# Optimization experiments

Measured on AMD Instinct MI355X. Metric: run time of the kernel, lower is better.

The kernel has to match this reference:

```python
import jax, jax.numpy as jnp
import numpy as np

N_ATOMS = 512
BATCH = 32


def _get_segments(n):
    # shifted pairs (k, k+1), all combinations of 2 rows, drop pairs where end1 == start2
    pairs = np.stack([np.arange(n - 1), np.arange(1, n)], axis=1)  # (n-1, 2)
    i, j = np.triu_indices(n - 1, k=1)
    seg = np.concatenate([pairs[i], pairs[j]], axis=1)  # (M, 4)
    seg = seg[seg[:, 1] != seg[:, 2]]
    return seg.astype(np.int32)  # (129795, 4) for n=512


def setup_inputs() -> dict:
    key = jax.random.key(0)
    x = jax.random.normal(key, (BATCH, N_ATOMS, 3), dtype=jnp.float32) * 5.0
    segments = jnp.asarray(_get_segments(N_ATOMS))
    return {"x": x, "segments": segments}


def _nnorm(v):
    return v / jnp.linalg.norm(v, axis=-1, keepdims=True)


def reference(x, segments):
    n = N_ATOMS
    x = x.reshape(-1, n, 3)
    B = x.shape[0]
    smat = x[:, segments]                       # (B, S, 4, 3) gather
    S = smat.shape[1]
    # displacements between the two segment endpoints pairs: d_{ab} = p_{2+b} - p_a
    disp = _nnorm((-smat[:, :, :2, None, :] + smat[:, :, None, 2:, :]).reshape(B, S, 4, 3))
    crosses = _nnorm(jnp.cross(disp[:, :, [0, 1, 3, 2]], disp[:, :, [1, 3, 2, 0]]))
    omega = jnp.arcsin(
        jnp.clip(jnp.sum(crosses * crosses[:, :, [1, 2, 3, 0]], axis=-1), -1.0, 1.0)
    ).sum(axis=2)                               # (B, S)
    signs = jnp.sign(
        jnp.sum(
            jnp.cross(_nnorm(smat[:, :, 3] - smat[:, :, 2]), _nnorm(smat[:, :, 1] - smat[:, :, 0]))
            * disp[:, :, 0],
            axis=-1,
        )
    )
    wr = (omega * signs) / (2.0 * jnp.pi)       # (B, S)
    # scatter into adjacency matrix (sequential sets: second overrides first, like torch)
    adj = jnp.zeros((B, n, n), dtype=x.dtype)
    adj = adj.at[:, segments[:, 0], segments[:, 2]].set(wr)
    adj = adj.at[:, segments[:, 1], segments[:, 3]].set(wr)
    return adj + jnp.swapaxes(adj, 1, 2)
```

## Files before the change

### kernel.cpp

```cpp
#include <hip/hip_runtime.h>
#include <math.h>

#define N 512
#define TILE 32
#define TSTRIDE 34
#define INV2PI 0.15915494309189535f

__device__ __forceinline__ float2 pset(float a, float b) { return make_float2(a, b); }
__device__ __forceinline__ float2 psplat(float a) { return make_float2(a, a); }
__device__ __forceinline__ float2 p_sub(float2 a, float2 b) { return make_float2(a.x - b.x, a.y - b.y); }
__device__ __forceinline__ float2 p_mul(float2 a, float2 b) { return make_float2(a.x * b.x, a.y * b.y); }
__device__ __forceinline__ float2 p_fma(float2 a, float2 b, float2 c) {
    return make_float2(fmaf(a.x, b.x, c.x), fmaf(a.y, b.y, c.y));
}
__device__ __forceinline__ float2 p_fmsub(float2 a, float2 b, float2 c, float2 d) {
    return make_float2(fmaf(a.x, b.x, -(c.x * d.x)), fmaf(a.y, b.y, -(c.y * d.y)));
}
__device__ __forceinline__ float2 p_rsq(float2 a) {
    return make_float2(__builtin_amdgcn_rsqf(a.x), __builtin_amdgcn_rsqf(a.y));
}

struct F3P { float2 x, y, z; };

__device__ __forceinline__ F3P pp_sub(F3P a, F3P b) {
    return {p_sub(a.x, b.x), p_sub(a.y, b.y), p_sub(a.z, b.z)};
}
__device__ __forceinline__ F3P pp_cross(F3P a, F3P b) {
    F3P c;
    c.x = p_fmsub(a.y, b.z, a.z, b.y);
    c.y = p_fmsub(a.z, b.x, a.x, b.z);
    c.z = p_fmsub(a.x, b.y, a.y, b.x);
    return c;
}
__device__ __forceinline__ float2 pp_dot(F3P a, F3P b) {
    return p_fma(a.x, b.x, p_fma(a.y, b.y, p_mul(a.z, b.z)));
}

__device__ __forceinline__ float2 p_asin_clamped(float2 t) {
    float2 ax = make_float2(fminf(fabsf(t.x), 1.f), fminf(fabsf(t.y), 1.f));
    float2 p = p_fma(ax, psplat(-0.0187293f), psplat(0.0742610f));
    p = p_fma(ax, p, psplat(-0.2121144f));
    p = p_fma(ax, p, psplat(1.5707288f));
    float sx = __builtin_amdgcn_sqrtf(1.0f - ax.x);
    float sy = __builtin_amdgcn_sqrtf(1.0f - ax.y);
    float rx = fmaf(-sx, p.x, 1.5707963267948966f);
    float ry = fmaf(-sy, p.y, 1.5707963267948966f);
    return make_float2(copysignf(rx, t.x), copysignf(ry, t.y));
}

__device__ __forceinline__ float2 wr_core2(F3P p0, F3P p1, F3P p2, F3P p3) {
    F3P u = pp_sub(p1, p0);
    F3P v = pp_sub(p3, p2);
    F3P d0 = pp_sub(p2, p0);

    F3P c0 = pp_cross(d0, v);
    F3P c3 = pp_cross(d0, u);
    F3P w  = pp_cross(u, v);
    F3P c1 = {p_sub(w.x, c3.x), p_sub(w.y, c3.y), p_sub(w.z, c3.z)};
    F3P c2 = {p_sub(w.x, c0.x), p_sub(w.y, c0.y), p_sub(w.z, c0.z)};

    float2 svn = pp_dot(w, d0);

    float2 q0 = pp_dot(c0, c0);
    float2 q1 = pp_dot(c1, c1);
    float2 q2 = pp_dot(c2, c2);
    float2 q3 = pp_dot(c3, c3);

    float2 t01 = p_mul(pp_dot(c0, c1), p_rsq(p_mul(q0, q1)));
    float2 t12 = p_mul(pp_dot(c1, c2), p_rsq(p_mul(q1, q2)));
    float2 t23 = p_mul(pp_dot(c2, c3), p_rsq(p_mul(q2, q3)));
    float2 t30 = p_mul(pp_dot(c3, c0), p_rsq(p_mul(q3, q0)));

    float2 a01 = p_asin_clamped(t01), a12 = p_asin_clamped(t12);
    float2 a23 = p_asin_clamped(t23), a30 = p_asin_clamped(t30);
    float2 omega = make_float2(a01.x + a12.x + a23.x + a30.x,
                               a01.y + a12.y + a23.y + a30.y);

    float ox = __int_as_float(__float_as_int(omega.x) ^
                              (__float_as_int(svn.x) & 0x80000000));
    float oy = __int_as_float(__float_as_int(omega.y) ^
                              (__float_as_int(svn.y) & 0x80000000));
    return make_float2(ox * -INV2PI, oy * -INV2PI);
}

__device__ __forceinline__ F3P pack_pt4(float4 a, float4 b) {
    F3P r;
    r.x = pset(a.x, b.x);
    r.y = pset(a.y, b.y);
    r.z = pset(a.z, b.z);
    return r;
}
__device__ __forceinline__ F3P pack_pt(const float4* __restrict__ xs4, int i0, int i1) {
    return pack_pt4(xs4[i0], xs4[i1]);
}
__device__ __forceinline__ F3P splat_pt(const float4* __restrict__ xs4, int i) {
    float4 a = xs4[i];
    F3P r;
    r.x = psplat(a.x);
    r.y = psplat(a.y);
    r.z = psplat(a.z);
    return r;
}

__device__ __forceinline__ void elem_idx(int gi, int gj, int& a, int& b, bool& valid) {
    const int lo = min(gi, gj), hi = max(gi, gj);
    const bool z = (lo == 0);
    a = z ? 0 : (lo - 1);
    b = z ? min(hi, 510) : (hi - 1);
    valid = z ? ((hi >= 2) && (hi <= 510)) : (hi >= lo + 2);
}

__global__ __launch_bounds__(256) void writhe_tile(const float* __restrict__ x,
                                                   float* __restrict__ out) {
    __shared__ __align__(16) float4 xs4[N];
    __shared__ __align__(16) float tsf[TILE * TSTRIDE];

    const int batch = blockIdx.y;

    {
        const float4* src = (const float4*)(x + (size_t)batch * (N * 3));
        float* xsf = (float*)xs4;
        for (int i = threadIdx.x; i < (N * 3) / 4; i += blockDim.x) {
            float4 g = src[i];
            const int base = 4 * i;
            float vv[4] = {g.x, g.y, g.z, g.w};
#pragma unroll
            for (int j = 0; j < 4; ++j) {
                const int e = base + j;
                xsf[(e / 3) * 4 + (e % 3)] = vv[j];
            }
        }
    }

    int p = blockIdx.x;
    int ti = 0;
    while (p >= (N / TILE) - ti) { p -= (N / TILE) - ti; ++ti; }
    const int tj = ti + p;
    const bool diag = (ti == tj);

    __syncthreads();

    float* ob = out + (size_t)batch * (N * N);

    if (ti >= 1 && !diag) {
        const int cp = threadIdx.x & 15;
        const int r = threadIdx.x >> 4;
        const int gj0 = tj * TILE + 2 * cp;

        const float4 qa = xs4[gj0 - 1];
        const float4 qb = xs4[gj0];
        const float4 qc = xs4[gj0 + 1];
        const F3P P2 = pack_pt4(qa, qb);
        const F3P P3 = pack_pt4(qb, qc);

#pragma unroll
        for (int k = 0; k < 2; ++k) {
            const int rr = r + 16 * k;
            const int gi = ti * TILE + rr;
            const F3P P0 = splat_pt(xs4, gi - 1);
            const F3P P1 = splat_pt(xs4, gi);
            float2 wr = wr_core2(P0, P1, P2, P3);
            const float vx = (gj0 >= gi + 2) ? wr.x : 0.f;
            const float vy = (gj0 + 1 >= gi + 2) ? wr.y : 0.f;
            const float2 vv = make_float2(vx, vy);
            *(float2*)(ob + (size_t)gi * N + gj0) = vv;
            *(float2*)(tsf + rr * TSTRIDE + 2 * cp) = vv;
        }

        __syncthreads();
        {
            const int r2 = threadIdx.x & 31;
            const int g = threadIdx.x >> 5;
            float4 o;
            o.x = tsf[(4 * g + 0) * TSTRIDE + r2];
            o.y = tsf[(4 * g + 1) * TSTRIDE + r2];
            o.z = tsf[(4 * g + 2) * TSTRIDE + r2];
            o.w = tsf[(4 * g + 3) * TSTRIDE + r2];
            *(float4*)(ob + (size_t)(tj * TILE + r2) * N + ti * TILE + 4 * g) = o;
        }
    } else {
        const int c = threadIdx.x & 31;
        const int r0 = threadIdx.x >> 5;
        const int gj = tj * TILE + c;

#pragma unroll
        for (int k = 0; k < 2; ++k) {
            const int rA = r0 + 8 * k;
            const int rB = rA + 16;
            const int giA = ti * TILE + rA;
            const int giB = ti * TILE + rB;

            int aA, bA, aB, bB;
            bool vA, vB;
            elem_idx(giA, gj, aA, bA, vA);
            elem_idx(giB, gj, aB, bB, vB);

            F3P P0 = pack_pt(xs4, aA, aB);
            F3P P1 = pack_pt(xs4, aA + 1, aB + 1);
            F3P P2 = pack_pt(xs4, bA, bB);
            F3P P3 = pack_pt(xs4, bA + 1, bB + 1);

            float2 wr = wr_core2(P0, P1, P2, P3);
            const float vxA = vA ? wr.x : 0.f;
            const float vxB = vB ? wr.y : 0.f;

            ob[(size_t)giA * N + gj] = vxA;
            ob[(size_t)giB * N + gj] = vxB;
            if (!diag) {
                tsf[rA * TSTRIDE + c] = vxA;
                tsf[rB * TSTRIDE + c] = vxB;
            }
        }

        if (!diag) {
            __syncthreads();
#pragma unroll
            for (int k = 0; k < 4; ++k) {
                const int r2 = r0 + 8 * k;
                ob[(size_t)(tj * TILE + r2) * N + (ti * TILE + c)] = tsf[c * TSTRIDE + r2];
            }
        }
    }
}

extern "C" void kernel_launch(void* const* d_in, const int* in_sizes, int n_in,
                              void* d_out, int out_size, void* d_ws, size_t ws_size,
                              hipStream_t stream) {
    const float* x = (const float*)d_in[0];
    float* out = (float*)d_out;
    const int B = in_sizes[0] / (N * 3);

    const int ntiles = N / TILE;
    const int npairs = ntiles * (ntiles + 1) / 2;

    dim3 block(256);
    dim3 grid(npairs, B);
    writhe_tile<<<grid, block, 0, stream>>>(x, out);
}
```

Before: 79.10 us.

## Halve block size to 128 threads, doubling per-thread rows and vectorising transpose stores

Shrinks the block from 256 to 128 threads, so each thread now computes four row pairs per tile instead of two. The off-diagonal path preloads all row points from shared memory ahead of the compute loop and drops the always-true validity mask on the second column. The diagonal and edge path now writes its transposed tile with float4 stores instead of scalar ones. This cuts the number of threads paying the per-block staging cost and widens the global stores, at the price of higher register pressure and less latency hiding per block.

```diff
diff --git a/kernel.cpp b/kernel.cpp
--- a/kernel.cpp
+++ b/kernel.cpp
@@ -93,8 +93,7 @@
 __device__ __forceinline__ F3P pack_pt(const float4* __restrict__ xs4, int i0, int i1) {
     return pack_pt4(xs4[i0], xs4[i1]);
 }
-__device__ __forceinline__ F3P splat_pt(const float4* __restrict__ xs4, int i) {
-    float4 a = xs4[i];
+__device__ __forceinline__ F3P splat_pt4(float4 a) {
     F3P r;
     r.x = psplat(a.x);
     r.y = psplat(a.y);
@@ -110,7 +109,7 @@
     valid = z ? ((hi >= 2) && (hi <= 510)) : (hi >= lo + 2);
 }
 
-__global__ __launch_bounds__(256) void writhe_tile(const float* __restrict__ x,
+__global__ __launch_bounds__(128) void writhe_tile(const float* __restrict__ x,
                                                    float* __restrict__ out) {
     __shared__ __align__(16) float4 xs4[N];
     __shared__ __align__(16) float tsf[TILE * TSTRIDE];
@@ -153,24 +152,30 @@
         const F3P P2 = pack_pt4(qa, qb);
         const F3P P3 = pack_pt4(qb, qc);
 
-#pragma unroll
-        for (int k = 0; k < 2; ++k) {
-            const int rr = r + 16 * k;
+        float4 ra[4], rb[4];
+#pragma unroll
+        for (int k = 0; k < 4; ++k) {
+            const int gi = ti * TILE + r + 8 * k;
+            ra[k] = xs4[gi - 1];
+            rb[k] = xs4[gi];
+        }
+
+#pragma unroll
+        for (int k = 0; k < 4; ++k) {
+            const int rr = r + 8 * k;
             const int gi = ti * TILE + rr;
-            const F3P P0 = splat_pt(xs4, gi - 1);
-            const F3P P1 = splat_pt(xs4, gi);
-            float2 wr = wr_core2(P0, P1, P2, P3);
+            float2 wr = wr_core2(splat_pt4(ra[k]), splat_pt4(rb[k]), P2, P3);
             const float vx = (gj0 >= gi + 2) ? wr.x : 0.f;
-            const float vy = (gj0 + 1 >= gi + 2) ? wr.y : 0.f;
-            const float2 vv = make_float2(vx, vy);
+            const float2 vv = make_float2(vx, wr.y);
             *(float2*)(ob + (size_t)gi * N + gj0) = vv;
             *(float2*)(tsf + rr * TSTRIDE + 2 * cp) = vv;
         }
 
         __syncthreads();
-        {
+#pragma unroll
+        for (int k = 0; k < 2; ++k) {
             const int r2 = threadIdx.x & 31;
-            const int g = threadIdx.x >> 5;
+            const int g = (threadIdx.x >> 5) + 4 * k;
             float4 o;
             o.x = tsf[(4 * g + 0) * TSTRIDE + r2];
             o.y = tsf[(4 * g + 1) * TSTRIDE + r2];
@@ -184,8 +189,8 @@
         const int gj = tj * TILE + c;
 
 #pragma unroll
-        for (int k = 0; k < 2; ++k) {
-            const int rA = r0 + 8 * k;
+        for (int k = 0; k < 4; ++k) {
+            const int rA = r0 + 4 * k;
             const int rB = rA + 16;
             const int giA = ti * TILE + rA;
             const int giB = ti * TILE + rB;
@@ -215,9 +220,15 @@
         if (!diag) {
             __syncthreads();
 #pragma unroll
-            for (int k = 0; k < 4; ++k) {
-                const int r2 = r0 + 8 * k;
-                ob[(size_t)(tj * TILE + r2) * N + (ti * TILE + c)] = tsf[c * TSTRIDE + r2];
+            for (int k = 0; k < 2; ++k) {
+                const int r2 = threadIdx.x & 31;
+                const int g = (threadIdx.x >> 5) + 4 * k;
+                float4 o;
+                o.x = tsf[(4 * g + 0) * TSTRIDE + r2];
+                o.y = tsf[(4 * g + 1) * TSTRIDE + r2];
+                o.z = tsf[(4 * g + 2) * TSTRIDE + r2];
+                o.w = tsf[(4 * g + 3) * TSTRIDE + r2];
+                *(float4*)(ob + (size_t)(tj * TILE + r2) * N + ti * TILE + 4 * g) = o;
             }
         }
     }
@@ -233,7 +244,7 @@
     const int ntiles = N / TILE;
     const int npairs = ntiles * (ntiles + 1) / 2;
 
-    dim3 block(256);
+    dim3 block(128);
     dim3 grid(npairs, B);
     writhe_tile<<<grid, block, 0, stream>>>(x, out);
 }
```

Result: slower. 81.28 us (+2.8%).
